# Kernel optimization log

Hardware: AMD Instinct MI355X
Metric: run time of the kernel (lower is better)

The kernel has to match this reference:

```python
import jax, jax.numpy as jnp
import numpy as np

B, Q, HID = 2, 2048, 2048
HQ, HKV, D = 16, 4, 128
EPS = 1e-6
THETA = 1000000.0


def _rmsnorm(x, w):
    # x: [..., D]
    return x * jax.lax.rsqrt(jnp.mean(x * x, axis=-1, keepdims=True) + EPS) * w


def _rope(x, cos, sin):
    # neox-style: split halves. x: [B,Q,H,D], cos/sin: [B,Q,1,D/2]
    d2 = x.shape[-1] // 2
    x1, x2 = x[..., :d2], x[..., d2:]
    return jnp.concatenate([x1 * cos - x2 * sin, x2 * cos + x1 * sin], axis=-1)


def setup_inputs() -> dict:
    key = jax.random.key(0)
    k1, k2, k3 = jax.random.split(key, 3)
    positions = jnp.broadcast_to(jnp.arange(Q, dtype=jnp.int32), (B, Q))
    hidden_states = jax.random.normal(k1, (B, Q, HID), dtype=jnp.float32)
    k_cache = jnp.zeros((B, HKV, Q, D), dtype=jnp.float32)
    v_cache = jnp.zeros((B, HKV, Q, D), dtype=jnp.float32)
    wqkv = jax.random.normal(k2, (HQ * D + 2 * HKV * D, HID), dtype=jnp.float32) * (HID ** -0.5)
    wo = jax.random.normal(k3, (HID, HQ * D), dtype=jnp.float32) * ((HQ * D) ** -0.5)
    q_norm_w = jnp.ones((D,), dtype=jnp.float32)
    k_norm_w = jnp.ones((D,), dtype=jnp.float32)
    return {"positions": positions, "hidden_states": hidden_states, "k_cache": k_cache,
            "v_cache": v_cache, "wqkv": wqkv, "wo": wo, "q_norm_w": q_norm_w,
            "k_norm_w": k_norm_w, "seq_len": Q}


def reference(positions, hidden_states, k_cache, v_cache, wqkv, wo, q_norm_w, k_norm_w, seq_len):
    bsz, qlen, _ = hidden_states.shape
    q_size, kv_size = HQ * D, HKV * D
    scale = D ** -0.5

    qkv = hidden_states.reshape(bsz * qlen, HID) @ wqkv.T  # [B*Q, q+2kv]
    q = qkv[:, :q_size].reshape(bsz, qlen, HQ, D)
    k = qkv[:, q_size:q_size + kv_size].reshape(bsz, qlen, HKV, D)
    v = qkv[:, q_size + kv_size:].reshape(bsz, qlen, HKV, D)

    q = _rmsnorm(q, q_norm_w)
    k = _rmsnorm(k, k_norm_w)

    inv_freq = 1.0 / (THETA ** (jnp.arange(0, D, 2, dtype=jnp.float32) / D))  # [D/2]
    freqs = positions.astype(jnp.float32)[..., None] * inv_freq  # [B,Q,D/2]
    cos = jnp.cos(freqs)[:, :, None, :]
    sin = jnp.sin(freqs)[:, :, None, :]
    q = _rope(q, cos, sin)
    k = _rope(k, cos, sin)

    q = q.transpose(0, 2, 1, 3)  # [B,HQ,Q,D]
    k = k.transpose(0, 2, 1, 3)  # [B,HKV,Q,D]
    v = v.transpose(0, 2, 1, 3)

    start = seq_len - qlen
    k_cache = jax.lax.dynamic_update_slice(k_cache, k, (0, 0, start, 0))
    v_cache = jax.lax.dynamic_update_slice(v_cache, v, (0, 0, start, 0))
    k_full = k_cache[:, :, :seq_len, :]
    v_full = v_cache[:, :, :seq_len, :]

    rep = HQ // HKV
    kf = jnp.repeat(k_full, rep, axis=1)  # [B,HQ,S,D]
    vf = jnp.repeat(v_full, rep, axis=1)

    scores = jnp.einsum('bhqd,bhkd->bhqk', q, kf) * scale
    if qlen == seq_len:  # is_causal path
        causal = jnp.tril(jnp.ones((qlen, seq_len), dtype=bool))
        scores = jnp.where(causal, scores, jnp.finfo(scores.dtype).min)
    attn = jax.nn.softmax(scores, axis=-1)
    out = jnp.einsum('bhqk,bhkd->bhqd', attn, vf)  # [B,HQ,Q,D]
    out = out.transpose(0, 2, 1, 3).reshape(bsz * qlen, HQ * D)
    return (out @ wo.T).reshape(bsz, qlen, HID)
```

## Files before the change

### kernel.cpp

```cpp
#include <hip/hip_runtime.h>

#define B_    2
#define Q_    2048
#define HID_  2048
#define HQ_   16
#define HKV_  4
#define D_    128
#define QSC_  (0.08838834764831843f * 1.4426950408889634f)
#define LOG2_THETA 19.931568569324174f
#define FMAX_ 20.0f

typedef unsigned short u16;
typedef __attribute__((ext_vector_type(8))) short bf16x8;
typedef __attribute__((ext_vector_type(4))) float f32x4;

__device__ __forceinline__ u16 f2bf(float x) {
  union { float f; unsigned int u; } v; v.f = x;
  unsigned int r = v.u + 0x7FFFu + ((v.u >> 16) & 1u);
  return (u16)(r >> 16);
}
__device__ __forceinline__ u16 f2bf_t(float x) {
  union { float f; unsigned int u; } v; v.f = x;
  return (u16)(v.u >> 16);
}

__device__ __forceinline__ void gl2lds16(u16* lds, const u16* g) {
  __builtin_amdgcn_global_load_lds((const __attribute__((address_space(1))) void*)g,
                                   (__attribute__((address_space(3))) void*)lds,
                                   16, 0, 0);
}

#define N4_HID  2097152
#define N4_WQKV 1572864
#define N4_WO   1048576
#define N4_ALL  (N4_HID + N4_WQKV + N4_WO)
#define NROPE   (B_ * Q_ * 64)
__global__ __launch_bounds__(256) void cvt_all(const float* __restrict__ h,
                                               const float* __restrict__ wq,
                                               const float* __restrict__ wo,
                                               const int* __restrict__ pos,
                                               u16* __restrict__ oh,
                                               u16* __restrict__ owq,
                                               u16* __restrict__ owo,
                                               float* __restrict__ rope) {
  int i = blockIdx.x * 256 + threadIdx.x;
  if (i >= N4_ALL) {
    int j = i - N4_ALL;
    int d = j & 63, row = j >> 6;
    float p = (float)pos[row];
    float inv = exp2f(-(float)d * (LOG2_THETA / 64.f));
    float sn, cn;
    sincosf(p * inv, &sn, &cn);
    ((float2*)rope)[j] = make_float2(cn, sn);
    return;
  }
  const float* src; u16* dst; int off;
  if (i < N4_HID)                 { src = h;  dst = oh;  off = i; }
  else if (i < N4_HID + N4_WQKV)  { src = wq; dst = owq; off = i - N4_HID; }
  else                            { src = wo; dst = owo; off = i - N4_HID - N4_WQKV; }
  float4 v = *(const float4*)(src + (size_t)off * 4);
  ushort4 o;
  o.x = f2bf(v.x); o.y = f2bf(v.y); o.z = f2bf(v.z); o.w = f2bf(v.w);
  *(ushort4*)(dst + (size_t)off * 4) = o;
}

__global__ __launch_bounds__(512) void gemm_qkv8(const u16* __restrict__ A,
                                                 const u16* __restrict__ Bw,
                                                 const float* __restrict__ rope,
                                                 const float* __restrict__ qw,
                                                 const float* __restrict__ kw,
                                                 u16* __restrict__ qb,
                                                 u16* __restrict__ kb,
                                                 u16* __restrict__ vt) {
  __shared__ __align__(16) u16 lds[65536];
  const int tid = threadIdx.x;
  const int wv = tid >> 6, lane = tid & 63;
  const int wm = wv >> 1, wn = wv & 1;
  const int c = lane & 15, quad = lane >> 4;
  const int m0 = blockIdx.x * 256;
  const int by = blockIdx.y;
  const int n0 = by * 256;
  const int xg = ((lane & 7) ^ (lane >> 3)) * 8;
  const int x0 = ((quad)     ^ (c & 7)) * 8;
  const int x1 = ((quad | 4) ^ (c & 7)) * 8;
  const int aoff = (wm >> 1) * 8192 + (wm & 1) * 4096 + c * 64;
  const int boff = 32768 + wn * 8192 + c * 64;
  const u16* Ag = A  + (size_t)m0 * HID_;
  const u16* Bg = Bw + (size_t)n0 * HID_;
  const int NIT = HID_ >> 7;

#define STGQ(base, g, h, kt, buf)                                             \
  { _Pragma("unroll")                                                         \
    for (int j = 0; j < 2; ++j) {                                             \
      const int s = j * 8 + wv;                                               \
      gl2lds16(lds + (base) + (buf) * 16384 + (h) * 8192 + s * 512,           \
               (g) + (size_t)((h) * 128 + s * 8 + (lane >> 3)) * HID_         \
                   + (kt) * 64 + xg);                                         \
    } }
#define STGQ_A(h, kt, buf) STGQ(0,     Ag, h, kt, buf)
#define STGQ_B(h, kt, buf) STGQ(32768, Bg, h, kt, buf)
#define BARQ()  asm volatile("s_barrier" ::: "memory")
#define WLGQ()  { asm volatile("s_waitcnt lgkmcnt(0)" ::: "memory");          \
                  __builtin_amdgcn_sched_barrier(0); }
#define WVMQ(n) { asm volatile("s_waitcnt vmcnt(" #n ")" ::: "memory");       \
                  __builtin_amdgcn_sched_barrier(0); }
#define MMQ(MF, NF, FA, MI) {                                                 \
  acc[MF][NF] = __builtin_amdgcn_mfma_f32_16x16x32_bf16(FA[MI][0], fB[(NF)&3][0], \
                                                        acc[MF][NF], 0, 0, 0);\
  acc[MF][NF] = __builtin_amdgcn_mfma_f32_16x16x32_bf16(FA[MI][1], fB[(NF)&3][1], \
                                                        acc[MF][NF], 0, 0, 0); }

  f32x4 acc[4][8] = {};
  bf16x8 fAa[2][2], fAb[2][2], fB[4][2];

  STGQ_A(0, 0, 0); STGQ_A(1, 0, 0); STGQ_B(0, 0, 0); STGQ_B(1, 0, 0);
  STGQ_A(0, 1, 1); STGQ_B(0, 1, 1);
  WVMQ(4);
  BARQ();

#pragma unroll 1
  for (int it = 0; it < NIT; ++it) {
    const bool last = (it == NIT - 1);
    const int kt1 = 2 * it + 1, kt2 = 2 * it + 2, kt3 = 2 * it + 3;

#pragma unroll
    for (int mi = 0; mi < 2; ++mi) {
      fAa[mi][0] = *(const bf16x8*)(lds + aoff + mi * 1024 + x0);
      fAa[mi][1] = *(const bf16x8*)(lds + aoff + mi * 1024 + x1);
    }
#pragma unroll
    for (int nf = 0; nf < 4; ++nf) {
      fB[nf][0] = *(const bf16x8*)(lds + boff + nf * 1024 + x0);
      fB[nf][1] = *(const bf16x8*)(lds + boff + nf * 1024 + x1);
    }
    STGQ_A(1, kt1, 1);
    BARQ(); WLGQ();
    __builtin_amdgcn_s_setprio(1);
#pragma unroll
    for (int mi = 0; mi < 2; ++mi)
#pragma unroll
      for (int nf = 0; nf < 4; ++nf) MMQ(mi, nf, fAa, mi);
    __builtin_amdgcn_s_setprio(0);
    BARQ();

#pragma unroll
    for (int mi = 0; mi < 2; ++mi) {
      fAb[mi][0] = *(const bf16x8*)(lds + aoff + (2 + mi) * 1024 + x0);
      fAb[mi][1] = *(const bf16x8*)(lds + aoff + (2 + mi) * 1024 + x1);
    }
    STGQ_B(1, kt1, 1);
    BARQ(); WLGQ();
    __builtin_amdgcn_s_setprio(1);
#pragma unroll
    for (int mi = 0; mi < 2; ++mi)
#pragma unroll
      for (int nf = 0; nf < 4; ++nf) MMQ(2 + mi, nf, fAb, mi);
    __builtin_amdgcn_s_setprio(0);
    BARQ();

#pragma unroll
    for (int nf = 0; nf < 4; ++nf) {
      fB[nf][0] = *(const bf16x8*)(lds + boff + (4 + nf) * 1024 + x0);
      fB[nf][1] = *(const bf16x8*)(lds + boff + (4 + nf) * 1024 + x1);
    }
    if (!last) STGQ_A(0, kt2, 0);
    BARQ(); WLGQ();
    __builtin_amdgcn_s_setprio(1);
#pragma unroll
    for (int mi = 0; mi < 2; ++mi)
#pragma unroll
      for (int nf = 4; nf < 8; ++nf) MMQ(2 + mi, nf, fAb, mi);
    __builtin_amdgcn_s_setprio(0);
    BARQ();

    if (!last) STGQ_B(0, kt2, 0);
    BARQ(); WLGQ();
    __builtin_amdgcn_s_setprio(1);
#pragma unroll
    for (int mi = 0; mi < 2; ++mi)
#pragma unroll
      for (int nf = 4; nf < 8; ++nf) MMQ(mi, nf, fAa, mi);
    __builtin_amdgcn_s_setprio(0);
    if (last) { WVMQ(0); } else { WVMQ(4); }
    BARQ();

#pragma unroll
    for (int mi = 0; mi < 2; ++mi) {
      fAa[mi][0] = *(const bf16x8*)(lds + 16384 + aoff + mi * 1024 + x0);
      fAa[mi][1] = *(const bf16x8*)(lds + 16384 + aoff + mi * 1024 + x1);
    }
#pragma unroll
    for (int nf = 0; nf < 4; ++nf) {
      fB[nf][0] = *(const bf16x8*)(lds + 16384 + boff + nf * 1024 + x0);
      fB[nf][1] = *(const bf16x8*)(lds + 16384 + boff + nf * 1024 + x1);
    }
    if (!last) STGQ_A(1, kt2, 0);
    BARQ(); WLGQ();
    __builtin_amdgcn_s_setprio(1);
#pragma unroll
    for (int mi = 0; mi < 2; ++mi)
#pragma unroll
      for (int nf = 0; nf < 4; ++nf) MMQ(mi, nf, fAa, mi);
    __builtin_amdgcn_s_setprio(0);
    BARQ();

#pragma unroll
    for (int mi = 0; mi < 2; ++mi) {
      fAb[mi][0] = *(const bf16x8*)(lds + 16384 + aoff + (2 + mi) * 1024 + x0);
      fAb[mi][1] = *(const bf16x8*)(lds + 16384 + aoff + (2 + mi) * 1024 + x1);
    }
    if (!last) STGQ_B(1, kt2, 0);
    BARQ(); WLGQ();
    __builtin_amdgcn_s_setprio(1);
#pragma unroll
    for (int mi = 0; mi < 2; ++mi)
#pragma unroll
      for (int nf = 0; nf < 4; ++nf) MMQ(2 + mi, nf, fAb, mi);
    __builtin_amdgcn_s_setprio(0);
    BARQ();

#pragma unroll
    for (int nf = 0; nf < 4; ++nf) {
      fB[nf][0] = *(const bf16x8*)(lds + 16384 + boff + (4 + nf) * 1024 + x0);
      fB[nf][1] = *(const bf16x8*)(lds + 16384 + boff + (4 + nf) * 1024 + x1);
    }
    if (!last) STGQ_A(0, kt3, 1);
    BARQ(); WLGQ();
    __builtin_amdgcn_s_setprio(1);
#pragma unroll
    for (int mi = 0; mi < 2; ++mi)
#pragma unroll
      for (int nf = 4; nf < 8; ++nf) MMQ(2 + mi, nf, fAb, mi);
    __builtin_amdgcn_s_setprio(0);
    BARQ();

    if (!last) STGQ_B(0, kt3, 1);
    BARQ(); WLGQ();
    __builtin_amdgcn_s_setprio(1);
#pragma unroll
    for (int mi = 0; mi < 2; ++mi)
#pragma unroll
      for (int nf = 4; nf < 8; ++nf) MMQ(mi, nf, fAa, mi);
    __builtin_amdgcn_s_setprio(0);
    if (last) { WVMQ(0); } else { WVMQ(4); }
    BARQ();
  }

  const int h = by * 2 + wn;
  if (h < 20) {
    const bool isq = h < 16;
    const float* w = isq ? qw : kw;
    const float osc = isq ? QSC_ : 1.f;
    float wl[8];
#pragma unroll
    for (int nf = 0; nf < 8; ++nf) wl[nf] = w[nf * 16 + c];
    u16* dstbuf = isq ? qb : kb;
    const int hbase = isq ? h : (h - 16);
    const int nheads = isq ? HQ_ : HKV_;
    u16* lw = lds + wv * 4224;
#pragma unroll
    for (int pass = 0; pass < 2; ++pass) {
#pragma unroll
      for (int mi = 0; mi < 2; ++mi) {
        const int mf = pass * 2 + mi;
#pragma unroll
        for (int r = 0; r < 4; ++r) {
          const int row = m0 + wm * 64 + mf * 16 + quad * 4 + r;
          const int q = row & (Q_ - 1), b = row >> 11;
          float ss = 0.f;
#pragma unroll
          for (int nf = 0; nf < 8; ++nf) ss += acc[mf][nf][r] * acc[mf][nf][r];
          ss += __shfl_xor(ss, 1); ss += __shfl_xor(ss, 2);
          ss += __shfl_xor(ss, 4); ss += __shfl_xor(ss, 8);
          const float rn = rsqrtf(ss * (1.f / 128.f) + 1e-6f) * osc;
          u16* lrow = lw + (mi * 16 + quad * 4 + r) * 132;
#pragma unroll
          for (int ni = 0; ni < 4; ni++) {
            float2 cssn = *(const float2*)(rope +
                ((size_t)(b * Q_ + q) * 64 + ni * 16 + c) * 2);
            float x1 = acc[mf][ni][r]     * wl[ni]     * rn;
            float x2 = acc[mf][ni + 4][r] * wl[ni + 4] * rn;
            lrow[ni * 16 + c]       = f2bf(x1 * cssn.x - x2 * cssn.y);
            lrow[(ni + 4) * 16 + c] = f2bf(x2 * cssn.x + x1 * cssn.y);
          }
        }
      }
#pragma unroll
      for (int itr = 0; itr < 8; ++itr) {
        const int rl = itr * 4 + quad;
        const int rowg = m0 + wm * 64 + pass * 32 + rl;
        const int q = rowg & (Q_ - 1), b = rowg >> 11;
        u16* dst = dstbuf + (((size_t)(b * nheads) + hbase) * Q_ + q) * D_ + c * 8;
        *(bf16x8*)dst = *(const bf16x8*)(lw + rl * 132 + c * 8);
      }
    }
  } else {
    const int hk = h - 20;
    const int bb = m0 >> 11;
    const int q0w = (m0 & (Q_ - 1)) + wm * 64;
    u16* lw = lds + wv * 4352;
#pragma unroll
    for (int pass = 0; pass < 2; ++pass) {
#pragma unroll
      for (int nfl = 0; nfl < 4; ++nfl) {
        const int nf = pass * 4 + nfl;
#pragma unroll
        for (int mf = 0; mf < 4; ++mf) {
          short4 pv;
          pv.x = (short)f2bf(acc[mf][nf][0]); pv.y = (short)f2bf(acc[mf][nf][1]);
          pv.z = (short)f2bf(acc[mf][nf][2]); pv.w = (short)f2bf(acc[mf][nf][3]);
          *(short4*)(lw + (nfl * 16 + c) * 68 + mf * 16 + quad * 4) = pv;
        }
      }
#pragma unroll
      for (int itr = 0; itr < 8; ++itr) {
        const int dl = itr * 8 + (lane >> 3);
        const int d = pass * 64 + dl;
        u16* dst = vt + (((size_t)(bb * HKV_) + hk) * D_ + d) * Q_ +
                   q0w + (lane & 7) * 8;
        *(bf16x8*)dst = *(const bf16x8*)(lw + dl * 68 + (lane & 7) * 8);
      }
    }
  }
#undef STGQ
#undef STGQ_A
#undef STGQ_B
#undef BARQ
#undef WLGQ
#undef WVMQ
#undef MMQ
}

__global__ __launch_bounds__(512) void gemm_bt8(const u16* __restrict__ A,
                                                const u16* __restrict__ Bw,
                                                float* __restrict__ C,
                                                int M, int N, int K) {
  __shared__ __align__(16) u16 lds[49152];
  const int tid = threadIdx.x;
  const int wv = tid >> 6, lane = tid & 63;
  const int wm = wv >> 2, wn = wv & 3;
  const int c = lane & 15, quad = lane >> 4;
  const int m0 = blockIdx.x * 128, n0 = blockIdx.y * 256;
  const int xg = ((lane & 7) ^ (lane >> 3)) * 8;
  const int x0 = ((quad)     ^ (c & 7)) * 8;
  const int x1 = ((quad | 4) ^ (c & 7)) * 8;
  const int aoff = wm * 4096 + c * 64;
  const int boff = 16384 + (wn >> 1) * 8192 + (wn & 1) * 4096 + c * 64;
  const u16* Ag = A  + (size_t)m0 * K;
  const u16* Bg = Bw + (size_t)n0 * K;
  const int NIT = K >> 7;

#define STA2(h, kt, buf)                                                      \
  gl2lds16(lds + (buf) * 8192 + (h) * 4096 + wv * 512,                        \
           Ag + (size_t)((h) * 64 + wv * 8 + (lane >> 3)) * K + (kt) * 64 + xg);
#define STB2(h, kt, buf)                                                      \
  { _Pragma("unroll")                                                         \
    for (int j = 0; j < 2; ++j)                                               \
      gl2lds16(lds + 16384 + (buf) * 16384 + (h) * 8192 + j * 4096 + wv * 512,\
               Bg + (size_t)((h) * 128 + j * 64 + wv * 8 + (lane >> 3)) * K   \
                   + (kt) * 64 + xg); }
#define BAR8()  asm volatile("s_barrier" ::: "memory")
#define WLG8()  { asm volatile("s_waitcnt lgkmcnt(0)" ::: "memory");          \
                  __builtin_amdgcn_sched_barrier(0); }
#define WVM8(n) { asm volatile("s_waitcnt vmcnt(" #n ")" ::: "memory");       \
                  __builtin_amdgcn_sched_barrier(0); }
#define MM2(MF, NF, FA, FB, MI, NI) {                                         \
  acc[MF][NF] = __builtin_amdgcn_mfma_f32_16x16x32_bf16(FA[MI][0], FB[NI][0], \
                                                        acc[MF][NF], 0, 0, 0);\
  acc[MF][NF] = __builtin_amdgcn_mfma_f32_16x16x32_bf16(FA[MI][1], FB[NI][1], \
                                                        acc[MF][NF], 0, 0, 0); }

  f32x4 acc[4][4] = {};
  bf16x8 fAa[2][2], fAb[2][2], fBa[2][2], fBb[2][2];

  STA2(0, 0, 0); STA2(1, 0, 0); STB2(0, 0, 0); STB2(1, 0, 0);
  STA2(0, 1, 1); STA2(1, 1, 1); STB2(0, 1, 1); STB2(1, 1, 1);
  WVM8(6);
  BAR8();

#pragma unroll 1
  for (int it = 0; it < NIT; ++it) {
    const bool last = (it == NIT - 1);
    const int kt2 = 2 * it + 2, kt3 = 2 * it + 3;

#pragma unroll
    for (int mi = 0; mi < 2; ++mi) {
      fAa[mi][0] = *(const bf16x8*)(lds + aoff + mi * 1024 + x0);
      fAa[mi][1] = *(const bf16x8*)(lds + aoff + mi * 1024 + x1);
      fBa[mi][0] = *(const bf16x8*)(lds + boff + mi * 1024 + x0);
      fBa[mi][1] = *(const bf16x8*)(lds + boff + mi * 1024 + x1);
    }
    BAR8(); WLG8();
    __builtin_amdgcn_s_setprio(1);
    MM2(0, 0, fAa, fBa, 0, 0); MM2(0, 1, fAa, fBa, 0, 1);
    MM2(1, 0, fAa, fBa, 1, 0); MM2(1, 1, fAa, fBa, 1, 1);
    __builtin_amdgcn_s_setprio(0);
    BAR8();

#pragma unroll
    for (int mi = 0; mi < 2; ++mi) {
      fAb[mi][0] = *(const bf16x8*)(lds + aoff + (2 + mi) * 1024 + x0);
      fAb[mi][1] = *(const bf16x8*)(lds + aoff + (2 + mi) * 1024 + x1);
    }
    BAR8(); WLG8();
    __builtin_amdgcn_s_setprio(1);
    MM2(2, 0, fAb, fBa, 0, 0); MM2(2, 1, fAb, fBa, 0, 1);
    MM2(3, 0, fAb, fBa, 1, 0); MM2(3, 1, fAb, fBa, 1, 1);
    __builtin_amdgcn_s_setprio(0);
    BAR8();

#pragma unroll
    for (int ni = 0; ni < 2; ++ni) {
      fBb[ni][0] = *(const bf16x8*)(lds + boff + (2 + ni) * 1024 + x0);
      fBb[ni][1] = *(const bf16x8*)(lds + boff + (2 + ni) * 1024 + x1);
    }
    if (!last) { STA2(0, kt2, 0); STA2(1, kt2, 0); }
    BAR8(); WLG8();
    __builtin_amdgcn_s_setprio(1);
    MM2(2, 2, fAb, fBb, 0, 0); MM2(2, 3, fAb, fBb, 0, 1);
    MM2(3, 2, fAb, fBb, 1, 0); MM2(3, 3, fAb, fBb, 1, 1);
    __builtin_amdgcn_s_setprio(0);
    BAR8();

    if (!last) { STB2(0, kt2, 0); STB2(1, kt2, 0); }
    BAR8(); WLG8();
    __builtin_amdgcn_s_setprio(1);
    MM2(0, 2, fAa, fBb, 0, 0); MM2(0, 3, fAa, fBb, 0, 1);
    MM2(1, 2, fAa, fBb, 1, 0); MM2(1, 3, fAa, fBb, 1, 1);
    __builtin_amdgcn_s_setprio(0);
    if (last) { WVM8(0); } else { WVM8(6); }
    BAR8();

#pragma unroll
    for (int mi = 0; mi < 2; ++mi) {
      fAa[mi][0] = *(const bf16x8*)(lds + 8192 + aoff + mi * 1024 + x0);
      fAa[mi][1] = *(const bf16x8*)(lds + 8192 + aoff + mi * 1024 + x1);
      fBa[mi][0] = *(const bf16x8*)(lds + 16384 + boff + mi * 1024 + x0);
      fBa[mi][1] = *(const bf16x8*)(lds + 16384 + boff + mi * 1024 + x1);
    }
    BAR8(); WLG8();
    __builtin_amdgcn_s_setprio(1);
    MM2(0, 0, fAa, fBa, 0, 0); MM2(0, 1, fAa, fBa, 0, 1);
    MM2(1, 0, fAa, fBa, 1, 0); MM2(1, 1, fAa, fBa, 1, 1);
    __builtin_amdgcn_s_setprio(0);
    BAR8();

#pragma unroll
    for (int mi = 0; mi < 2; ++mi) {
      fAb[mi][0] = *(const bf16x8*)(lds + 8192 + aoff + (2 + mi) * 1024 + x0);
      fAb[mi][1] = *(const bf16x8*)(lds + 8192 + aoff + (2 + mi) * 1024 + x1);
    }
    BAR8(); WLG8();
    __builtin_amdgcn_s_setprio(1);
    MM2(2, 0, fAb, fBa, 0, 0); MM2(2, 1, fAb, fBa, 0, 1);
    MM2(3, 0, fAb, fBa, 1, 0); MM2(3, 1, fAb, fBa, 1, 1);
    __builtin_amdgcn_s_setprio(0);
    BAR8();

#pragma unroll
    for (int ni = 0; ni < 2; ++ni) {
      fBb[ni][0] = *(const bf16x8*)(lds + 16384 + boff + (2 + ni) * 1024 + x0);
      fBb[ni][1] = *(const bf16x8*)(lds + 16384 + boff + (2 + ni) * 1024 + x1);
    }
    if (!last) { STA2(0, kt3, 1); STA2(1, kt3, 1); }
    BAR8(); WLG8();
    __builtin_amdgcn_s_setprio(1);
    MM2(2, 2, fAb, fBb, 0, 0); MM2(2, 3, fAb, fBb, 0, 1);
    MM2(3, 2, fAb, fBb, 1, 0); MM2(3, 3, fAb, fBb, 1, 1);
    __builtin_amdgcn_s_setprio(0);
    BAR8();

    if (!last) { STB2(0, kt3, 1); STB2(1, kt3, 1); }
    BAR8(); WLG8();
    __builtin_amdgcn_s_setprio(1);
    MM2(0, 2, fAa, fBb, 0, 0); MM2(0, 3, fAa, fBb, 0, 1);
    MM2(1, 2, fAa, fBb, 1, 0); MM2(1, 3, fAa, fBb, 1, 1);
    __builtin_amdgcn_s_setprio(0);
    if (last) { WVM8(0); } else { WVM8(6); }
    BAR8();
  }

  const int crow = m0 + wm * 64 + quad * 4;
  const int ccol = n0 + wn * 64 + c;
#pragma unroll
  for (int mf = 0; mf < 4; ++mf)
#pragma unroll
    for (int nf = 0; nf < 4; ++nf)
#pragma unroll
      for (int r = 0; r < 4; ++r)
        C[(size_t)(crow + mf * 16 + r) * N + ccol + nf * 16] = acc[mf][nf][r];
#undef STA2
#undef STB2
#undef BAR8
#undef WLG8
#undef WVM8
#undef MM2
}

__global__ __launch_bounds__(256) void attn_fwd(const u16* __restrict__ qb,
                                                const u16* __restrict__ kb,
                                                const u16* __restrict__ vt,
                                                u16* __restrict__ ob) {
  __shared__ __align__(16) u16 lds[2 * 8192 + 2 * 8192 + 4608];
  const int p = blockIdx.x, h = blockIdx.y, b = blockIdx.z;
  const int hk = h >> 2;
  const int tid = threadIdx.x, wave = tid >> 6, lane = tid & 63;
  const int c = lane & 15, quad = lane >> 4;
  const int lr = lane >> 2, lp = lane & 3;
  const int lpg = (lp + 4 - ((lr >> 1) & 3)) & 3;
  const int swq = ((quad + (c >> 1)) & 3) * 8;
  const u16* qg = qb + ((size_t)b * HQ_ + h) * (size_t)Q_ * D_;
  const u16* kg = kb + ((size_t)b * HKV_ + hk) * (size_t)Q_ * D_;
  const u16* vg = vt + ((size_t)b * HKV_ + hk) * (size_t)D_ * Q_;
  u16* Pw = lds + 32768 + wave * 1152;
  u16* Bw = lds + wave * 2176;

#define ASTAGE(KT, BS)                                                        \
  { _Pragma("unroll")                                                         \
    for (int i = 0; i < 4; i++) {                                             \
      gl2lds16(lds + (BS) * 8192 + (size_t)(i * 256 + wave * 64) * 8,         \
               kg + ((size_t)(KT) * 64 + wave * 16 + lr) * D_ + i * 32 + lpg * 8); \
      int d = (i & 1) * 64 + wave * 16 + lr;                                  \
      gl2lds16(lds + 16384 + (BS) * 8192 + (size_t)(i * 256 + wave * 64) * 8, \
               vg + (size_t)d * Q_ + (KT) * 64 + (i >> 1) * 32 + lpg * 8);    \
    } }

#pragma unroll 1
  for (int tp = 0; tp < 2; tp++) {
    const int t = tp ? (31 - p) : p;
    const int q0 = t * 64;
    const int qrow = q0 + wave * 16 + c;
    bf16x8 qf[4];
#pragma unroll
    for (int kk = 0; kk < 4; kk++)
      qf[kk] = *(const bf16x8*)(qg + (size_t)qrow * D_ + kk * 32 + quad * 8);
    f32x4 Oa[8] = {};
    float l_acc = 0.f;

    if (tp) __syncthreads();
    ASTAGE(0, 0);

#pragma unroll 1
    for (int kt = 0; kt <= t; kt++) {
      const int bs = kt & 1;
      __syncthreads();
      if (kt < t) ASTAGE(kt + 1, bs ^ 1);
      const u16* Ksb = lds + bs * 8192;
      const u16* Vsb = lds + 16384 + bs * 8192;
      f32x4 S[4];
#pragma unroll
      for (int n = 0; n < 4; n++) {
        f32x4 a = {-FMAX_, -FMAX_, -FMAX_, -FMAX_};
#pragma unroll
        for (int kk = 0; kk < 4; kk++) {
          bf16x8 kf = *(const bf16x8*)(Ksb + kk * 2048 + (n * 16 + c) * 32 + swq);
          a = __builtin_amdgcn_mfma_f32_16x16x32_bf16(kf, qf[kk], a, 0, 0, 0);
        }
        S[n] = a;
      }
      if (kt == t) {
#pragma unroll
        for (int n = 0; n < 4; n++)
#pragma unroll
          for (int r = 0; r < 4; r++) {
            int key = kt * 64 + n * 16 + quad * 4 + r;
            if (key > qrow) S[n][r] = -1e9f;
          }
      }
#pragma unroll
      for (int n = 0; n < 4; n++) {
        float p0 = __builtin_amdgcn_exp2f(S[n][0]);
        float p1 = __builtin_amdgcn_exp2f(S[n][1]);
        float p2 = __builtin_amdgcn_exp2f(S[n][2]);
        float p3 = __builtin_amdgcn_exp2f(S[n][3]);
        l_acc += (p0 + p1) + (p2 + p3);
        short4 pk;
        pk.x = (short)f2bf_t(p0); pk.y = (short)f2bf_t(p1);
        pk.z = (short)f2bf_t(p2); pk.w = (short)f2bf_t(p3);
        *(short4*)(Pw + c * 72 + n * 16 + quad * 4) = pk;
      }
      bf16x8 pf[2];
#pragma unroll
      for (int kk2 = 0; kk2 < 2; kk2++)
        pf[kk2] = *(const bf16x8*)(Pw + c * 72 + kk2 * 32 + quad * 8);
#pragma unroll
      for (int md = 0; md < 8; md++)
#pragma unroll
        for (int kk2 = 0; kk2 < 2; kk2++) {
          bf16x8 vf = *(const bf16x8*)(Vsb + kk2 * 4096 + (md * 16 + c) * 32 + swq);
          Oa[md] = __builtin_amdgcn_mfma_f32_16x16x32_bf16(vf, pf[kk2], Oa[md], 0, 0, 0);
        }
    }
    float l_row = l_acc;
    l_row += __shfl_xor(l_row, 16);
    l_row += __shfl_xor(l_row, 32);
    __syncthreads();
    const float invl = 1.f / l_row;
#pragma unroll
    for (int md = 0; md < 8; md++) {
      short4 ok;
      ok.x = (short)f2bf(Oa[md][0] * invl); ok.y = (short)f2bf(Oa[md][1] * invl);
      ok.z = (short)f2bf(Oa[md][2] * invl); ok.w = (short)f2bf(Oa[md][3] * invl);
      *(short4*)(Bw + c * 136 + md * 16 + quad * 4) = ok;
    }
    const int orow = q0 + wave * 16 + lr;
#pragma unroll
    for (int tt = 0; tt < 4; tt++) {
      bf16x8 ov = *(const bf16x8*)(Bw + lr * 136 + lp * 32 + tt * 8);
      *(bf16x8*)(ob + ((size_t)(b * Q_ + orow) * HQ_ + h) * D_ + lp * 32 + tt * 8) = ov;
    }
  }
#undef ASTAGE
}

extern "C" void kernel_launch(void* const* d_in, const int* in_sizes, int n_in,
                              void* d_out, int out_size, void* d_ws, size_t ws_size,
                              hipStream_t stream) {
  const int*   positions = (const int*)  d_in[0];
  const float* hidden    = (const float*)d_in[1];
  const float* wqkv      = (const float*)d_in[4];
  const float* wo        = (const float*)d_in[5];
  const float* qnw       = (const float*)d_in[6];
  const float* knw       = (const float*)d_in[7];
  char* ws = (char*)d_ws;
  u16*   hid_bf  = (u16*)(ws);
  u16*   wqkv_bf = (u16*)(ws + 16777216);
  u16*   wo_bf   = (u16*)(ws + 29360128);
  u16*   q_bf    = (u16*)(ws + 37748736);
  u16*   k_bf    = (u16*)(ws + 54525952);
  u16*   vt_bf   = (u16*)(ws + 58720256);
  float* rope    = (float*)(ws + 62914560);
  u16*   attn_bf = hid_bf;

  cvt_all<<<19456, 256, 0, stream>>>(hidden, wqkv, wo, positions,
                                     hid_bf, wqkv_bf, wo_bf, rope);
  gemm_qkv8<<<dim3(16, 12), 512, 0, stream>>>(hid_bf, wqkv_bf, rope, qnw, knw,
                                              q_bf, k_bf, vt_bf);
  attn_fwd<<<dim3(16, 16, 2), 256, 0, stream>>>(q_bf, k_bf, vt_bf, attn_bf);
  gemm_bt8<<<dim3(32, 8), 512, 0, stream>>>(attn_bf, wo_bf, (float*)d_out,
                                            4096, 2048, 2048);
}
```

Measured before the change: 281.5 us.

## Process two 16-row query sub-tiles per wave in causal attention

Each wave now handles 32 query rows (two 16-row halves) instead of 16, so one workgroup covers a 128-row query tile. Every K/V fragment read from LDS is reused for two MFMAs, which halves K/V staging traffic per query row. The grid shrinks to 8x16x2 blocks (256 total), which lowers parallelism and roughly doubles register pressure from the accumulators. The causal mask now covers the last two key tiles.

```diff
diff --git a/kernel.cpp b/kernel.cpp
--- a/kernel.cpp
+++ b/kernel.cpp
@@ -501,7 +501,7 @@
                                                 const u16* __restrict__ kb,
                                                 const u16* __restrict__ vt,
                                                 u16* __restrict__ ob) {
-  __shared__ __align__(16) u16 lds[2 * 8192 + 2 * 8192 + 4608];
+  __shared__ __align__(16) u16 lds[32768 + 9216];
   const int p = blockIdx.x, h = blockIdx.y, b = blockIdx.z;
   const int hk = h >> 2;
   const int tid = threadIdx.x, wave = tid >> 6, lane = tid & 63;
@@ -512,7 +512,7 @@
   const u16* qg = qb + ((size_t)b * HQ_ + h) * (size_t)Q_ * D_;
   const u16* kg = kb + ((size_t)b * HKV_ + hk) * (size_t)Q_ * D_;
   const u16* vg = vt + ((size_t)b * HKV_ + hk) * (size_t)D_ * Q_;
-  u16* Pw = lds + 32768 + wave * 1152;
+  u16* Pw = lds + 32768 + wave * 2304;
   u16* Bw = lds + wave * 2176;
 
 #define ASTAGE(KT, BS)                                                        \
@@ -524,93 +524,115 @@
       gl2lds16(lds + 16384 + (BS) * 8192 + (size_t)(i * 256 + wave * 64) * 8, \
                vg + (size_t)d * Q_ + (KT) * 64 + (i >> 1) * 32 + lpg * 8);    \
     } }
+#define MFMA_A(A0, B0, C0) __builtin_amdgcn_mfma_f32_16x16x32_bf16(A0, B0, C0, 0, 0, 0)
 
 #pragma unroll 1
   for (int tp = 0; tp < 2; tp++) {
-    const int t = tp ? (31 - p) : p;
-    const int q0 = t * 64;
-    const int qrow = q0 + wave * 16 + c;
-    bf16x8 qf[4];
-#pragma unroll
-    for (int kk = 0; kk < 4; kk++)
-      qf[kk] = *(const bf16x8*)(qg + (size_t)qrow * D_ + kk * 32 + quad * 8);
-    f32x4 Oa[8] = {};
-    float l_acc = 0.f;
+    const int t = tp ? (15 - p) : p;
+    const int q0 = t * 128;
+    const int qbase = q0 + wave * 32;
+    bf16x8 qf[2][4];
+#pragma unroll
+    for (int qh = 0; qh < 2; qh++)
+#pragma unroll
+      for (int kk = 0; kk < 4; kk++)
+        qf[qh][kk] = *(const bf16x8*)(qg + (size_t)(qbase + qh * 16 + c) * D_ +
+                                      kk * 32 + quad * 8);
+    f32x4 Oa[8][2] = {};
+    float l0 = 0.f, l1 = 0.f;
 
     if (tp) __syncthreads();
     ASTAGE(0, 0);
 
+    const int nkt = 2 * t + 2;
 #pragma unroll 1
-    for (int kt = 0; kt <= t; kt++) {
+    for (int kt = 0; kt < nkt; kt++) {
       const int bs = kt & 1;
       __syncthreads();
-      if (kt < t) ASTAGE(kt + 1, bs ^ 1);
+      if (kt < nkt - 1) ASTAGE(kt + 1, bs ^ 1);
       const u16* Ksb = lds + bs * 8192;
       const u16* Vsb = lds + 16384 + bs * 8192;
-      f32x4 S[4];
+      f32x4 S[4][2];
 #pragma unroll
       for (int n = 0; n < 4; n++) {
-        f32x4 a = {-FMAX_, -FMAX_, -FMAX_, -FMAX_};
+        S[n][0] = f32x4{-FMAX_, -FMAX_, -FMAX_, -FMAX_};
+        S[n][1] = f32x4{-FMAX_, -FMAX_, -FMAX_, -FMAX_};
 #pragma unroll
         for (int kk = 0; kk < 4; kk++) {
           bf16x8 kf = *(const bf16x8*)(Ksb + kk * 2048 + (n * 16 + c) * 32 + swq);
-          a = __builtin_amdgcn_mfma_f32_16x16x32_bf16(kf, qf[kk], a, 0, 0, 0);
+          S[n][0] = MFMA_A(kf, qf[0][kk], S[n][0]);
+          S[n][1] = MFMA_A(kf, qf[1][kk], S[n][1]);
         }
-        S[n] = a;
-      }
-      if (kt == t) {
+      }
+      if (kt >= 2 * t) {
 #pragma unroll
         for (int n = 0; n < 4; n++)
 #pragma unroll
-          for (int r = 0; r < 4; r++) {
-            int key = kt * 64 + n * 16 + quad * 4 + r;
-            if (key > qrow) S[n][r] = -1e9f;
-          }
-      }
-#pragma unroll
-      for (int n = 0; n < 4; n++) {
-        float p0 = __builtin_amdgcn_exp2f(S[n][0]);
-        float p1 = __builtin_amdgcn_exp2f(S[n][1]);
-        float p2 = __builtin_amdgcn_exp2f(S[n][2]);
-        float p3 = __builtin_amdgcn_exp2f(S[n][3]);
-        l_acc += (p0 + p1) + (p2 + p3);
-        short4 pk;
-        pk.x = (short)f2bf_t(p0); pk.y = (short)f2bf_t(p1);
-        pk.z = (short)f2bf_t(p2); pk.w = (short)f2bf_t(p3);
-        *(short4*)(Pw + c * 72 + n * 16 + quad * 4) = pk;
-      }
-      bf16x8 pf[2];
-#pragma unroll
-      for (int kk2 = 0; kk2 < 2; kk2++)
-        pf[kk2] = *(const bf16x8*)(Pw + c * 72 + kk2 * 32 + quad * 8);
+          for (int qh = 0; qh < 2; qh++)
+#pragma unroll
+            for (int r = 0; r < 4; r++) {
+              int key = kt * 64 + n * 16 + quad * 4 + r;
+              if (key > qbase + qh * 16 + c) S[n][qh][r] = -1e9f;
+            }
+      }
+#pragma unroll
+      for (int n = 0; n < 4; n++)
+#pragma unroll
+        for (int qh = 0; qh < 2; qh++) {
+          float p0 = __builtin_amdgcn_exp2f(S[n][qh][0]);
+          float p1 = __builtin_amdgcn_exp2f(S[n][qh][1]);
+          float p2 = __builtin_amdgcn_exp2f(S[n][qh][2]);
+          float p3 = __builtin_amdgcn_exp2f(S[n][qh][3]);
+          if (qh) l1 += (p0 + p1) + (p2 + p3);
+          else    l0 += (p0 + p1) + (p2 + p3);
+          short4 pk;
+          pk.x = (short)f2bf_t(p0); pk.y = (short)f2bf_t(p1);
+          pk.z = (short)f2bf_t(p2); pk.w = (short)f2bf_t(p3);
+          *(short4*)(Pw + (qh * 16 + c) * 72 + n * 16 + quad * 4) = pk;
+        }
+      bf16x8 pf[2][2];
+#pragma unroll
+      for (int qh = 0; qh < 2; qh++)
+#pragma unroll
+        for (int kk2 = 0; kk2 < 2; kk2++)
+          pf[qh][kk2] = *(const bf16x8*)(Pw + (qh * 16 + c) * 72 +
+                                         kk2 * 32 + quad * 8);
 #pragma unroll
       for (int md = 0; md < 8; md++)
 #pragma unroll
         for (int kk2 = 0; kk2 < 2; kk2++) {
           bf16x8 vf = *(const bf16x8*)(Vsb + kk2 * 4096 + (md * 16 + c) * 32 + swq);
-          Oa[md] = __builtin_amdgcn_mfma_f32_16x16x32_bf16(vf, pf[kk2], Oa[md], 0, 0, 0);
+          Oa[md][0] = MFMA_A(vf, pf[0][kk2], Oa[md][0]);
+          Oa[md][1] = MFMA_A(vf, pf[1][kk2], Oa[md][1]);
         }
     }
-    float l_row = l_acc;
-    l_row += __shfl_xor(l_row, 16);
-    l_row += __shfl_xor(l_row, 32);
+    l0 += __shfl_xor(l0, 16); l0 += __shfl_xor(l0, 32);
+    l1 += __shfl_xor(l1, 16); l1 += __shfl_xor(l1, 32);
     __syncthreads();
-    const float invl = 1.f / l_row;
-#pragma unroll
-    for (int md = 0; md < 8; md++) {
-      short4 ok;
-      ok.x = (short)f2bf(Oa[md][0] * invl); ok.y = (short)f2bf(Oa[md][1] * invl);
-      ok.z = (short)f2bf(Oa[md][2] * invl); ok.w = (short)f2bf(Oa[md][3] * invl);
-      *(short4*)(Bw + c * 136 + md * 16 + quad * 4) = ok;
-    }
-    const int orow = q0 + wave * 16 + lr;
-#pragma unroll
-    for (int tt = 0; tt < 4; tt++) {
-      bf16x8 ov = *(const bf16x8*)(Bw + lr * 136 + lp * 32 + tt * 8);
-      *(bf16x8*)(ob + ((size_t)(b * Q_ + orow) * HQ_ + h) * D_ + lp * 32 + tt * 8) = ov;
+#pragma unroll
+    for (int qh = 0; qh < 2; qh++) {
+      const float invl = 1.f / (qh ? l1 : l0);
+#pragma unroll
+      for (int md = 0; md < 8; md++) {
+        short4 ok;
+        ok.x = (short)f2bf(Oa[md][qh][0] * invl);
+        ok.y = (short)f2bf(Oa[md][qh][1] * invl);
+        ok.z = (short)f2bf(Oa[md][qh][2] * invl);
+        ok.w = (short)f2bf(Oa[md][qh][3] * invl);
+        *(short4*)(Bw + c * 136 + md * 16 + quad * 4) = ok;
+      }
+      const int orow = q0 + wave * 32 + qh * 16 + lr;
+#pragma unroll
+      for (int tt = 0; tt < 4; tt++) {
+        bf16x8 ov = *(const bf16x8*)(Bw + lr * 136 + lp * 32 + tt * 8);
+        *(bf16x8*)(ob + ((size_t)(b * Q_ + orow) * HQ_ + h) * D_ + lp * 32 + tt * 8) = ov;
+      }
+      asm volatile("s_waitcnt lgkmcnt(0)" ::: "memory");
+      __builtin_amdgcn_sched_barrier(0);
     }
   }
 #undef ASTAGE
+#undef MFMA_A
 }
 
 extern "C" void kernel_launch(void* const* d_in, const int* in_sizes, int n_in,
@@ -636,7 +658,7 @@
                                      hid_bf, wqkv_bf, wo_bf, rope);
   gemm_qkv8<<<dim3(16, 12), 512, 0, stream>>>(hid_bf, wqkv_bf, rope, qnw, knw,
                                               q_bf, k_bf, vt_bf);
-  attn_fwd<<<dim3(16, 16, 2), 256, 0, stream>>>(q_bf, k_bf, vt_bf, attn_bf);
+  attn_fwd<<<dim3(8, 16, 2), 256, 0, stream>>>(q_bf, k_bf, vt_bf, attn_bf);
   gemm_bt8<<<dim3(32, 8), 512, 0, stream>>>(attn_bf, wo_bf, (float*)d_out,
                                             4096, 2048, 2048);
 }
```

Result: slower. 287.8 us (+2.2%).
